# Optimization experiments

Hardware: AMD Instinct MI355X
Metric: run time of the kernel (lower is better)

Reference implementation:

```python
import jax, jax.numpy as jnp
import numpy as np


def setup_inputs() -> dict:
    key = jax.random.key(0)
    ks = jax.random.split(key, 6)
    B, S, D, H, K = 16384, 16, 256, 128, 32
    s1 = 1.0 / np.sqrt(D)
    s2 = 1.0 / np.sqrt(H)
    s3 = 1.0 / np.sqrt(K)
    return {
        "x": jax.random.normal(ks[0], (B, D), jnp.float32),
        "W1": jax.random.normal(ks[1], (S, D, H), jnp.float32) * s1,
        "b1": jnp.zeros((S, H), jnp.float32),
        "W2": jax.random.normal(ks[2], (S, H, D), jnp.float32) * s2,
        "b2": jnp.zeros((S, D), jnp.float32),
        "Wc1": jax.random.normal(ks[3], (S, D, K), jnp.float32) * s1,
        "bc1": jnp.zeros((S, K), jnp.float32),
        "Wc2": jax.random.normal(ks[4], (S, K), jnp.float32) * s3,
        "bc2": jnp.zeros((S,), jnp.float32),
        "lam": jnp.ones((S,), jnp.float32) / S,  # lambda_weights init = 1/n_sources
    }


def reference(x, W1, b1, W2, b2, Wc1, bc1, Wc2, bc2, lam):
    # Batched per-source 2-layer MLP: [B,D] x [S,D,H] -> [B,S,H]
    h = jax.nn.relu(jnp.einsum("bd,sdh->bsh", x, W1) + b1[None])
    outs = jnp.einsum("bsh,shd->bsd", h, W2) + b2[None]            # [B,S,D]
    # Confidence net on each source output
    ch = jax.nn.relu(jnp.einsum("bsd,sdk->bsk", outs, Wc1) + bc1[None])
    conf = jax.nn.sigmoid(jnp.einsum("bsk,sk->bs", ch, Wc2) + bc2[None])  # [B,S]
    # Weighted, normalized combination
    cw = lam[None, :] * conf                                        # [B,S]
    cw = cw / (cw.sum(axis=1, keepdims=True) + 1e-6)
    out = jnp.einsum("bsd,bs->bd", outs, cw)                        # [B,D]
    return out
```

## Files before the change

### kernel.cpp

```cpp
#include <hip/hip_runtime.h>
#include <math.h>

#define S_N 16
#define D_N 256
#define H_N 128
#define K_N 32
#define BT  64
#define B_N 16384

typedef __attribute__((ext_vector_type(8))) short bf16x8;
typedef __attribute__((ext_vector_type(4))) short bf16x4;
typedef __attribute__((ext_vector_type(4))) float f32x4;
typedef __attribute__((ext_vector_type(16))) float f32x16;

#define MFMA16(a, b, c) __builtin_amdgcn_mfma_f32_16x16x32_bf16(a, b, c, 0, 0, 0)
#define MFMA32(a, b, c) __builtin_amdgcn_mfma_f32_32x32x16_bf16(a, b, c, 0, 0, 0)
#define SWZ(r) ((unsigned)(((r) & 15) << 4))

static __device__ __forceinline__ unsigned short f2bf(float f) {
  union { float f; unsigned u; } v; v.f = f;
  unsigned r = v.u + 0x7FFFu + ((v.u >> 16) & 1u);
  return (unsigned short)(r >> 16);
}

__global__ __launch_bounds__(256)
void lsi_prep(const float* __restrict__ W1, const float* __restrict__ W2,
              const float* __restrict__ Wc1, const float* __restrict__ b2,
              const float* __restrict__ bc1,
              unsigned short* __restrict__ W1t,
              unsigned short* __restrict__ W2t,
              unsigned short* __restrict__ Wft,
              float* __restrict__ bcf)
{
  const int bid = blockIdx.x;
  if (bid < 1024) {
    __shared__ float t[32][33];
    const float* src; unsigned short* dst; int R, C, r0, c0;
    if (bid < 512) {
      int s = bid >> 5, tt = bid & 31;
      R = 256; C = 128; r0 = (tt >> 2) * 32; c0 = (tt & 3) * 32;
      src = W1 + (size_t)s * 256 * 128; dst = W1t + (size_t)s * 128 * 256;
    } else {
      int s = (bid - 512) >> 5, tt = (bid - 512) & 31;
      R = 128; C = 256; r0 = (tt >> 3) * 32; c0 = (tt & 7) * 32;
      src = W2 + (size_t)s * 128 * 256; dst = W2t + (size_t)s * 256 * 128;
    }
    int li = threadIdx.x >> 5, lj = threadIdx.x & 31;
    #pragma unroll
    for (int i = 0; i < 4; ++i)
      t[li + i * 8][lj] = src[(size_t)(r0 + li + i * 8) * C + c0 + lj];
    __syncthreads();
    #pragma unroll
    for (int i = 0; i < 4; ++i)
      dst[(size_t)(c0 + li + i * 8) * R + r0 + lj] = f2bf(t[lj][li + i * 8]);
    return;
  }
  const int q  = bid - 1024;
  const int s  = q >> 3, hb = q & 7;
  const int t  = threadIdx.x;
  const int hh = hb * 16 + (t >> 4);
  const int kb = (t & 15) * 2;
  const float* w2r = W2 + ((size_t)s * H_N + hh) * D_N;
  const float* wc1 = Wc1 + (size_t)s * D_N * K_N;
  float a0 = 0.f, a1 = 0.f;
  for (int d = 0; d < D_N; ++d) {
    float wv = w2r[d];
    a0 = fmaf(wv, wc1[d * K_N + kb], a0);
    a1 = fmaf(wv, wc1[d * K_N + kb + 1], a1);
  }
  Wft[((size_t)s * K_N + kb) * H_N + hh]     = f2bf(a0);
  Wft[((size_t)s * K_N + kb + 1) * H_N + hh] = f2bf(a1);
  if (hb == 0 && t < K_N) {
    float a = bc1[s * K_N + t];
    for (int d = 0; d < D_N; ++d)
      a = fmaf(b2[s * D_N + d], wc1[d * K_N + t], a);
    bcf[s * K_N + t] = a;
  }
}

__global__ __launch_bounds__(512, 2)
void lsi_main(const float* __restrict__ x,
              const float* __restrict__ b1,
              const float* __restrict__ b2,
              const float* __restrict__ Wc2,
              const float* __restrict__ bc2,
              const float* __restrict__ lam,
              const unsigned short* __restrict__ W1t,
              const unsigned short* __restrict__ W2t,
              const unsigned short* __restrict__ Wft,
              const float* __restrict__ bcf,
              float* __restrict__ out)
{
  __shared__ __align__(16) unsigned short x_lds[BT * D_N];
  __shared__ __align__(16) unsigned short h_lds[2][BT * H_N];
  __shared__ float cw_lds[2][BT];
  __shared__ float wsum_lds[BT];

  const int tid = threadIdx.x;
  const int w   = tid >> 6;
  const int l   = tid & 63;
  const int l31 = l & 31;
  const int hi  = l >> 5;
  const int l15 = l & 15;
  const int g   = l >> 4;
  const int b0  = blockIdx.x * BT;
  const int bt1 = w >> 2;
  const int ct1 = w & 3;

  {
    int row = tid >> 3;
    int c0  = (tid & 7) * 32;
    const float* xr = x + (size_t)(b0 + row) * D_N + c0;
    #pragma unroll
    for (int cc = 0; cc < 4; ++cc) {
      float4 f0 = *(const float4*)(xr + cc * 8);
      float4 f1 = *(const float4*)(xr + cc * 8 + 4);
      bf16x8 u;
      u[0] = f2bf(f0.x); u[1] = f2bf(f0.y); u[2] = f2bf(f0.z); u[3] = f2bf(f0.w);
      u[4] = f2bf(f1.x); u[5] = f2bf(f1.y); u[6] = f2bf(f1.z); u[7] = f2bf(f1.w);
      unsigned off = (unsigned)(row * 512 + (c0 + cc * 8) * 2) ^ SWZ(row);
      *(bf16x8*)((char*)x_lds + off) = u;
    }
  }
  if (tid < BT) wsum_lds[tid] = 0.f;

  f32x16 out_acc[2], acc2[2];
  #pragma unroll
  for (int i = 0; i < 16; ++i) {
    out_acc[0][i] = 0.f; out_acc[1][i] = 0.f;
  }

  auto do_gemm1 = [&](int s, unsigned short* hw) {
    const int brow = bt1 * 32 + l31;
    f32x16 a1a, a1b;
    #pragma unroll
    for (int i = 0; i < 16; ++i) { a1a[i] = 0.f; a1b[i] = 0.f; }
    const unsigned short* A1 = W1t + ((size_t)s * H_N + ct1 * 32 + l31) * D_N + hi * 8;
    const unsigned xbase = (unsigned)(brow * 512 + hi * 16);
    #pragma unroll
    for (int kf = 0; kf < 16; kf += 2) {
      bf16x8 aw0 = *(const bf16x8*)(A1 + kf * 16);
      bf16x8 aw1 = *(const bf16x8*)(A1 + kf * 16 + 16);
      bf16x8 bx0 = *(const bf16x8*)((const char*)x_lds + ((xbase + kf * 32) ^ SWZ(brow)));
      bf16x8 bx1 = *(const bf16x8*)((const char*)x_lds + ((xbase + kf * 32 + 32) ^ SWZ(brow)));
      a1a = MFMA32(aw0, bx0, a1a);
      a1b = MFMA32(aw1, bx1, a1b);
    }
    #pragma unroll
    for (int q = 0; q < 4; ++q) {
      f32x4 b4 = *(const f32x4*)(b1 + s * H_N + ct1 * 32 + q * 8 + hi * 4);
      bf16x4 hv;
      #pragma unroll
      for (int i = 0; i < 4; ++i)
        hv[i] = (short)f2bf(fmaxf(a1a[q * 4 + i] + a1b[q * 4 + i] + b4[i], 0.f));
      unsigned off = (unsigned)(brow * 256 + (ct1 * 32 + q * 8 + hi * 4) * 2) ^ SWZ(brow);
      *(bf16x4*)((char*)hw + off) = hv;
    }
  };

  __syncthreads();
  do_gemm1(0, h_lds[0]);
  __syncthreads();

  for (int s = 0; s < S_N; ++s) {
    const unsigned short* hr = (const unsigned short*)h_lds[s & 1];

    if (s > 0) {
      float cw0 = cw_lds[(s - 1) & 1][l31];
      float cw1 = cw_lds[(s - 1) & 1][32 + l31];
      #pragma unroll
      for (int r = 0; r < 16; ++r) {
        out_acc[0][r] += cw0 * acc2[0][r];
        out_acc[1][r] += cw1 * acc2[1][r];
      }
    }

    if (s + 1 < S_N) do_gemm1(s + 1, h_lds[(s + 1) & 1]);

    if (w < 4) {
      const int crow = w * 16 + l15;
      f32x4 c3a = (f32x4){0.f, 0.f, 0.f, 0.f};
      f32x4 c3b = (f32x4){0.f, 0.f, 0.f, 0.f};
      const unsigned short* Af = Wft + ((size_t)s * K_N + l15) * H_N + g * 8;
      const unsigned cb = (unsigned)(crow * 256 + g * 16);
      #pragma unroll
      for (int ks = 0; ks < 4; ++ks) {
        bf16x8 hb = *(const bf16x8*)((const char*)hr + ((cb + ks * 64) ^ SWZ(crow)));
        c3a = MFMA16(*(const bf16x8*)(Af + ks * 32), hb, c3a);
        c3b = MFMA16(*(const bf16x8*)(Af + 16 * H_N + ks * 32), hb, c3b);
      }
      float zz = 0.f;
      {
        f32x4 bcf4 = *(const f32x4*)(bcf + s * K_N + g * 4);
        f32x4 wc4  = *(const f32x4*)(Wc2 + s * K_N + g * 4);
        #pragma unroll
        for (int i = 0; i < 4; ++i)
          zz += fmaxf(c3a[i] + bcf4[i], 0.f) * wc4[i];
        bcf4 = *(const f32x4*)(bcf + s * K_N + 16 + g * 4);
        wc4  = *(const f32x4*)(Wc2 + s * K_N + 16 + g * 4);
        #pragma unroll
        for (int i = 0; i < 4; ++i)
          zz += fmaxf(c3b[i] + bcf4[i], 0.f) * wc4[i];
      }
      zz += __shfl_xor(zz, 16);
      zz += __shfl_xor(zz, 32);
      if (l < 16) {
        float cv = lam[s] / (1.f + __expf(-(zz + bc2[s])));
        cw_lds[s & 1][w * 16 + l] = cv;
        wsum_lds[w * 16 + l] += cv;
      }
    }

    #pragma unroll
    for (int i = 0; i < 16; ++i) { acc2[0][i] = 0.f; acc2[1][i] = 0.f; }
    {
      const unsigned short* A2 = W2t + ((size_t)s * D_N + w * 32 + l31) * H_N + hi * 8;
      const unsigned hb0 = (unsigned)(l31 * 256 + hi * 16);
      const unsigned hb1 = (unsigned)((32 + l31) * 256 + hi * 16);
      #pragma unroll
      for (int kf = 0; kf < 8; ++kf) {
        bf16x8 aw = *(const bf16x8*)(A2 + kf * 16);
        bf16x8 h0 = *(const bf16x8*)((const char*)hr + ((hb0 + kf * 32) ^ SWZ(l31)));
        bf16x8 h1 = *(const bf16x8*)((const char*)hr + ((hb1 + kf * 32) ^ SWZ(l31)));
        acc2[0] = MFMA32(aw, h0, acc2[0]);
        acc2[1] = MFMA32(aw, h1, acc2[1]);
      }
      #pragma unroll
      for (int q = 0; q < 4; ++q) {
        f32x4 b24 = *(const f32x4*)(b2 + s * D_N + w * 32 + q * 8 + hi * 4);
        #pragma unroll
        for (int i = 0; i < 4; ++i) {
          acc2[0][q * 4 + i] += b24[i];
          acc2[1][q * 4 + i] += b24[i];
        }
      }
    }
    __syncthreads();
  }

  {
    float cw0 = cw_lds[(S_N - 1) & 1][l31];
    float cw1 = cw_lds[(S_N - 1) & 1][32 + l31];
    float wi0 = 1.f / (wsum_lds[l31] + 1e-6f);
    float wi1 = 1.f / (wsum_lds[32 + l31] + 1e-6f);
    #pragma unroll
    for (int r = 0; r < 16; ++r) {
      out_acc[0][r] = (out_acc[0][r] + cw0 * acc2[0][r]) * wi0;
      out_acc[1][r] = (out_acc[1][r] + cw1 * acc2[1][r]) * wi1;
    }
  }
  {
    float* tb = (w < 4 ? (float*)x_lds : (float*)h_lds) + (w & 3) * 1152;
    #pragma unroll
    for (int t = 0; t < 2; ++t) {
      __syncthreads();
      #pragma unroll
      for (int q = 0; q < 4; ++q) {
        f32x4 v;
        #pragma unroll
        for (int i = 0; i < 4; ++i) v[i] = out_acc[t][q * 4 + i];
        *(f32x4*)(tb + l31 * 36 + q * 8 + hi * 4) = v;
      }
      __syncthreads();
      #pragma unroll
      for (int p = 0; p < 2; ++p) {
        int row = (l >> 2) + p * 16;
        f32x4 v0 = *(const f32x4*)(tb + row * 36 + (l & 3) * 8);
        f32x4 v1 = *(const f32x4*)(tb + row * 36 + (l & 3) * 8 + 4);
        float* op = out + (size_t)(b0 + t * 32 + row) * D_N + w * 32 + (l & 3) * 8;
        *(f32x4*)op = v0;
        *(f32x4*)(op + 4) = v1;
      }
    }
  }
}

extern "C" void kernel_launch(void* const* d_in, const int* in_sizes, int n_in,
                              void* d_out, int out_size, void* d_ws, size_t ws_size,
                              hipStream_t stream) {
  const float* x   = (const float*)d_in[0];
  const float* W1  = (const float*)d_in[1];
  const float* b1  = (const float*)d_in[2];
  const float* W2  = (const float*)d_in[3];
  const float* b2  = (const float*)d_in[4];
  const float* Wc1 = (const float*)d_in[5];
  const float* bc1 = (const float*)d_in[6];
  const float* Wc2 = (const float*)d_in[7];
  const float* bc2 = (const float*)d_in[8];
  const float* lam = (const float*)d_in[9];
  float* out = (float*)d_out;

  unsigned short* W1t = (unsigned short*)d_ws;
  unsigned short* W2t = W1t + (size_t)S_N * H_N * D_N;
  unsigned short* Wft = W2t + (size_t)S_N * D_N * H_N;
  float* bcf = (float*)(Wft + (size_t)S_N * K_N * H_N);

  lsi_prep<<<dim3(1152), dim3(256), 0, stream>>>(W1, W2, Wc1, b2, bc1,
                                                 W1t, W2t, Wft, bcf);
  lsi_main<<<dim3(B_N / BT), dim3(512), 0, stream>>>(x, b1, b2, Wc2, bc2, lam,
                                                     W1t, W2t, Wft, bcf, out);
}
```

Before: 137.8 us.

## Fold confidence weights into hidden activations and split sources across two blocks

Scales the hidden activations h by each row's confidence weight before the second GEMM, so the weighted sum over sources accumulates straight into the MFMA output instead of through a separate FMA pass. The b2 bias contribution is added once at the end using stored per-source weights. Tiles shrink to 32 rows with 256-thread blocks, and when workspace allows, the 16 sources are split across two blocks whose partial sums and weight totals are merged by a new combine kernel. This gives more parallelism and occupancy, at the cost of an extra bf16 rounding of the scaled h, extra barriers per source, and the write and read of two full fp32 partial outputs.

```diff
diff --git a/kernel.cpp b/kernel.cpp
--- a/kernel.cpp
+++ b/kernel.cpp
@@ -5,7 +5,7 @@
 #define D_N 256
 #define H_N 128
 #define K_N 32
-#define BT  64
+#define BT  32
 #define B_N 16384
 
 typedef __attribute__((ext_vector_type(8))) short bf16x8;
@@ -21,6 +21,10 @@
   union { float f; unsigned u; } v; v.f = f;
   unsigned r = v.u + 0x7FFFu + ((v.u >> 16) & 1u);
   return (unsigned short)(r >> 16);
+}
+static __device__ __forceinline__ float bf2f(unsigned short u) {
+  union { unsigned u; float f; } v; v.u = ((unsigned)u) << 16;
+  return v.f;
 }
 
 __global__ __launch_bounds__(256)
@@ -78,7 +82,8 @@
   }
 }
 
-__global__ __launch_bounds__(512, 2)
+template<int SPLIT>
+__global__ __launch_bounds__(256, 4)
 void lsi_main(const float* __restrict__ x,
               const float* __restrict__ b1,
               const float* __restrict__ b2,
@@ -89,11 +94,13 @@
               const unsigned short* __restrict__ W2t,
               const unsigned short* __restrict__ Wft,
               const float* __restrict__ bcf,
-              float* __restrict__ out)
+              float* __restrict__ outp,
+              float* __restrict__ pwsum)
 {
   __shared__ __align__(16) unsigned short x_lds[BT * D_N];
   __shared__ __align__(16) unsigned short h_lds[2][BT * H_N];
-  __shared__ float cw_lds[2][BT];
+  __shared__ float zp_lds[2][BT];
+  __shared__ float cwh[16][BT];
   __shared__ float wsum_lds[BT];
 
   const int tid = threadIdx.x;
@@ -103,9 +110,11 @@
   const int hi  = l >> 5;
   const int l15 = l & 15;
   const int g   = l >> 4;
-  const int b0  = blockIdx.x * BT;
-  const int bt1 = w >> 2;
-  const int ct1 = w & 3;
+
+  int rb, half, s0, ns;
+  if (SPLIT) { rb = blockIdx.x & 511; half = blockIdx.x >> 9; s0 = half * 8; ns = 8; }
+  else       { rb = blockIdx.x;       half = 0;               s0 = 0;        ns = 16; }
+  const int b0 = rb * BT;
 
   {
     int row = tid >> 3;
@@ -124,141 +133,135 @@
   }
   if (tid < BT) wsum_lds[tid] = 0.f;
 
-  f32x16 out_acc[2], acc2[2];
+  f32x16 oa0, oa1;
   #pragma unroll
-  for (int i = 0; i < 16; ++i) {
-    out_acc[0][i] = 0.f; out_acc[1][i] = 0.f;
-  }
+  for (int i = 0; i < 16; ++i) { oa0[i] = 0.f; oa1[i] = 0.f; }
 
   auto do_gemm1 = [&](int s, unsigned short* hw) {
-    const int brow = bt1 * 32 + l31;
-    f32x16 a1a, a1b;
-    #pragma unroll
-    for (int i = 0; i < 16; ++i) { a1a[i] = 0.f; a1b[i] = 0.f; }
-    const unsigned short* A1 = W1t + ((size_t)s * H_N + ct1 * 32 + l31) * D_N + hi * 8;
-    const unsigned xbase = (unsigned)(brow * 512 + hi * 16);
-    #pragma unroll
-    for (int kf = 0; kf < 16; kf += 2) {
-      bf16x8 aw0 = *(const bf16x8*)(A1 + kf * 16);
-      bf16x8 aw1 = *(const bf16x8*)(A1 + kf * 16 + 16);
-      bf16x8 bx0 = *(const bf16x8*)((const char*)x_lds + ((xbase + kf * 32) ^ SWZ(brow)));
-      bf16x8 bx1 = *(const bf16x8*)((const char*)x_lds + ((xbase + kf * 32 + 32) ^ SWZ(brow)));
-      a1a = MFMA32(aw0, bx0, a1a);
-      a1b = MFMA32(aw1, bx1, a1b);
+    f32x16 a1;
+    #pragma unroll
+    for (int i = 0; i < 16; ++i) a1[i] = 0.f;
+    const unsigned short* A1 = W1t + ((size_t)s * H_N + w * 32 + l31) * D_N + hi * 8;
+    #pragma unroll
+    for (int kf = 0; kf < 16; ++kf) {
+      bf16x8 aw = *(const bf16x8*)(A1 + kf * 16);
+      bf16x8 bx = *(const bf16x8*)((const char*)x_lds +
+                    ((unsigned)(l31 * 512 + kf * 32 + hi * 16) ^ SWZ(l31)));
+      a1 = MFMA32(aw, bx, a1);
     }
     #pragma unroll
     for (int q = 0; q < 4; ++q) {
-      f32x4 b4 = *(const f32x4*)(b1 + s * H_N + ct1 * 32 + q * 8 + hi * 4);
+      f32x4 b4 = *(const f32x4*)(b1 + s * H_N + w * 32 + q * 8 + hi * 4);
       bf16x4 hv;
       #pragma unroll
       for (int i = 0; i < 4; ++i)
-        hv[i] = (short)f2bf(fmaxf(a1a[q * 4 + i] + a1b[q * 4 + i] + b4[i], 0.f));
-      unsigned off = (unsigned)(brow * 256 + (ct1 * 32 + q * 8 + hi * 4) * 2) ^ SWZ(brow);
+        hv[i] = (short)f2bf(fmaxf(a1[q * 4 + i] + b4[i], 0.f));
+      unsigned off = (unsigned)(l31 * 256 + (w * 32 + q * 8 + hi * 4) * 2) ^ SWZ(l31);
       *(bf16x4*)((char*)hw + off) = hv;
     }
   };
 
   __syncthreads();
-  do_gemm1(0, h_lds[0]);
+  do_gemm1(s0, h_lds[0]);
   __syncthreads();
 
-  for (int s = 0; s < S_N; ++s) {
-    const unsigned short* hr = (const unsigned short*)h_lds[s & 1];
-
-    if (s > 0) {
-      float cw0 = cw_lds[(s - 1) & 1][l31];
-      float cw1 = cw_lds[(s - 1) & 1][32 + l31];
-      #pragma unroll
-      for (int r = 0; r < 16; ++r) {
-        out_acc[0][r] += cw0 * acc2[0][r];
-        out_acc[1][r] += cw1 * acc2[1][r];
-      }
-    }
-
-    if (s + 1 < S_N) do_gemm1(s + 1, h_lds[(s + 1) & 1]);
-
-    if (w < 4) {
-      const int crow = w * 16 + l15;
-      f32x4 c3a = (f32x4){0.f, 0.f, 0.f, 0.f};
-      f32x4 c3b = (f32x4){0.f, 0.f, 0.f, 0.f};
-      const unsigned short* Af = Wft + ((size_t)s * K_N + l15) * H_N + g * 8;
-      const unsigned cb = (unsigned)(crow * 256 + g * 16);
+  for (int si = 0; si < ns; ++si) {
+    const int s = s0 + si;
+    const unsigned short* hr = (const unsigned short*)h_lds[si & 1];
+
+    if (si + 1 < ns) do_gemm1(s + 1, h_lds[(si + 1) & 1]);
+    {
+      const int bt = w >> 1, kt = w & 1;
+      f32x4 c3 = (f32x4){0.f, 0.f, 0.f, 0.f};
+      const unsigned short* Af = Wft + ((size_t)s * K_N + kt * 16 + l15) * H_N + g * 8;
       #pragma unroll
       for (int ks = 0; ks < 4; ++ks) {
-        bf16x8 hb = *(const bf16x8*)((const char*)hr + ((cb + ks * 64) ^ SWZ(crow)));
-        c3a = MFMA16(*(const bf16x8*)(Af + ks * 32), hb, c3a);
-        c3b = MFMA16(*(const bf16x8*)(Af + 16 * H_N + ks * 32), hb, c3b);
-      }
+        int brow = bt * 16 + l15;
+        bf16x8 hb = *(const bf16x8*)((const char*)hr +
+                      ((unsigned)(brow * 256 + ks * 64 + g * 16) ^ SWZ(brow)));
+        c3 = MFMA16(*(const bf16x8*)(Af + ks * 32), hb, c3);
+      }
+      f32x4 bc4 = *(const f32x4*)(bcf + s * K_N + kt * 16 + g * 4);
+      f32x4 wc4 = *(const f32x4*)(Wc2 + s * K_N + kt * 16 + g * 4);
       float zz = 0.f;
-      {
-        f32x4 bcf4 = *(const f32x4*)(bcf + s * K_N + g * 4);
-        f32x4 wc4  = *(const f32x4*)(Wc2 + s * K_N + g * 4);
-        #pragma unroll
-        for (int i = 0; i < 4; ++i)
-          zz += fmaxf(c3a[i] + bcf4[i], 0.f) * wc4[i];
-        bcf4 = *(const f32x4*)(bcf + s * K_N + 16 + g * 4);
-        wc4  = *(const f32x4*)(Wc2 + s * K_N + 16 + g * 4);
-        #pragma unroll
-        for (int i = 0; i < 4; ++i)
-          zz += fmaxf(c3b[i] + bcf4[i], 0.f) * wc4[i];
-      }
+      #pragma unroll
+      for (int i = 0; i < 4; ++i)
+        zz += fmaxf(c3[i] + bc4[i], 0.f) * wc4[i];
       zz += __shfl_xor(zz, 16);
       zz += __shfl_xor(zz, 32);
-      if (l < 16) {
-        float cv = lam[s] / (1.f + __expf(-(zz + bc2[s])));
-        cw_lds[s & 1][w * 16 + l] = cv;
-        wsum_lds[w * 16 + l] += cv;
-      }
-    }
-
-    #pragma unroll
-    for (int i = 0; i < 16; ++i) { acc2[0][i] = 0.f; acc2[1][i] = 0.f; }
+      if (l < 16) zp_lds[kt][bt * 16 + l] = zz;
+    }
+    __syncthreads();
+
     {
-      const unsigned short* A2 = W2t + ((size_t)s * D_N + w * 32 + l31) * H_N + hi * 8;
-      const unsigned hb0 = (unsigned)(l31 * 256 + hi * 16);
-      const unsigned hb1 = (unsigned)((32 + l31) * 256 + hi * 16);
+      unsigned short* hm = h_lds[si & 1];
+      const int r  = tid >> 3;
+      const int c0 = (tid & 7) * 32;
+      float cv = lam[s] / (1.f + __expf(-(zp_lds[0][r] + zp_lds[1][r] + bc2[s])));
+      unsigned off0 = (unsigned)(r * 256 + c0) ^ SWZ(r);
+      unsigned off1 = (unsigned)(r * 256 + c0 + 16) ^ SWZ(r);
+      bf16x8 v0 = *(const bf16x8*)((const char*)hm + off0);
+      bf16x8 v1 = *(const bf16x8*)((const char*)hm + off1);
+      #pragma unroll
+      for (int j = 0; j < 8; ++j) {
+        v0[j] = (short)f2bf(bf2f((unsigned short)v0[j]) * cv);
+        v1[j] = (short)f2bf(bf2f((unsigned short)v1[j]) * cv);
+      }
+      *(bf16x8*)((char*)hm + off0) = v0;
+      *(bf16x8*)((char*)hm + off1) = v1;
+      if ((tid & 7) == 0) {
+        wsum_lds[r] += cv;
+        cwh[si][r] = cv;
+      }
+    }
+    __syncthreads();
+
+    {
+      const unsigned short* A2 = W2t + ((size_t)s * D_N + w * 64 + l31) * H_N + hi * 8;
       #pragma unroll
       for (int kf = 0; kf < 8; ++kf) {
-        bf16x8 aw = *(const bf16x8*)(A2 + kf * 16);
-        bf16x8 h0 = *(const bf16x8*)((const char*)hr + ((hb0 + kf * 32) ^ SWZ(l31)));
-        bf16x8 h1 = *(const bf16x8*)((const char*)hr + ((hb1 + kf * 32) ^ SWZ(l31)));
-        acc2[0] = MFMA32(aw, h0, acc2[0]);
-        acc2[1] = MFMA32(aw, h1, acc2[1]);
-      }
-      #pragma unroll
-      for (int q = 0; q < 4; ++q) {
-        f32x4 b24 = *(const f32x4*)(b2 + s * D_N + w * 32 + q * 8 + hi * 4);
-        #pragma unroll
-        for (int i = 0; i < 4; ++i) {
-          acc2[0][q * 4 + i] += b24[i];
-          acc2[1][q * 4 + i] += b24[i];
-        }
+        bf16x8 hb = *(const bf16x8*)((const char*)hr +
+                      ((unsigned)(l31 * 256 + kf * 32 + hi * 16) ^ SWZ(l31)));
+        oa0 = MFMA32(*(const bf16x8*)(A2 + kf * 16), hb, oa0);
+        oa1 = MFMA32(*(const bf16x8*)(A2 + 32 * H_N + kf * 16), hb, oa1);
       }
     }
     __syncthreads();
   }
 
+  #pragma unroll
+  for (int q = 0; q < 4; ++q) {
+    const int dc0 = w * 64 + q * 8 + hi * 4;
+    for (int si = 0; si < ns; ++si) {
+      const float c = cwh[si][l31];
+      f32x4 ba = *(const f32x4*)(b2 + (s0 + si) * D_N + dc0);
+      f32x4 bb = *(const f32x4*)(b2 + (s0 + si) * D_N + dc0 + 32);
+      #pragma unroll
+      for (int i = 0; i < 4; ++i) {
+        oa0[q * 4 + i] += c * ba[i];
+        oa1[q * 4 + i] += c * bb[i];
+      }
+    }
+  }
+  if (!SPLIT) {
+    const float winv = 1.f / (wsum_lds[l31] + 1e-6f);
+    #pragma unroll
+    for (int i = 0; i < 16; ++i) { oa0[i] *= winv; oa1[i] *= winv; }
+  }
+
   {
-    float cw0 = cw_lds[(S_N - 1) & 1][l31];
-    float cw1 = cw_lds[(S_N - 1) & 1][32 + l31];
-    float wi0 = 1.f / (wsum_lds[l31] + 1e-6f);
-    float wi1 = 1.f / (wsum_lds[32 + l31] + 1e-6f);
-    #pragma unroll
-    for (int r = 0; r < 16; ++r) {
-      out_acc[0][r] = (out_acc[0][r] + cw0 * acc2[0][r]) * wi0;
-      out_acc[1][r] = (out_acc[1][r] + cw1 * acc2[1][r]) * wi1;
-    }
-  }
-  {
-    float* tb = (w < 4 ? (float*)x_lds : (float*)h_lds) + (w & 3) * 1152;
-    #pragma unroll
-    for (int t = 0; t < 2; ++t) {
+    float* tb = (w < 2) ? ((float*)x_lds + w * 1152)
+                        : ((float*)h_lds + (w - 2) * 1152);
+    float* po = outp + (SPLIT ? (size_t)half * B_N * D_N : 0);
+    #pragma unroll
+    for (int ct = 0; ct < 2; ++ct) {
       __syncthreads();
       #pragma unroll
       for (int q = 0; q < 4; ++q) {
         f32x4 v;
         #pragma unroll
-        for (int i = 0; i < 4; ++i) v[i] = out_acc[t][q * 4 + i];
+        for (int i = 0; i < 4; ++i)
+          v[i] = ct ? oa1[q * 4 + i] : oa0[q * 4 + i];
         *(f32x4*)(tb + l31 * 36 + q * 8 + hi * 4) = v;
       }
       __syncthreads();
@@ -267,12 +270,29 @@
         int row = (l >> 2) + p * 16;
         f32x4 v0 = *(const f32x4*)(tb + row * 36 + (l & 3) * 8);
         f32x4 v1 = *(const f32x4*)(tb + row * 36 + (l & 3) * 8 + 4);
-        float* op = out + (size_t)(b0 + t * 32 + row) * D_N + w * 32 + (l & 3) * 8;
+        float* op = po + (size_t)(b0 + row) * D_N + w * 64 + ct * 32 + (l & 3) * 8;
         *(f32x4*)op = v0;
         *(f32x4*)(op + 4) = v1;
       }
     }
   }
+  if (SPLIT && tid < BT) pwsum[half * B_N + b0 + tid] = wsum_lds[tid];
+}
+
+__global__ __launch_bounds__(256)
+void lsi_combine(const float* __restrict__ pout, const float* __restrict__ pwsum,
+                 float* __restrict__ out)
+{
+  size_t i4 = ((size_t)blockIdx.x * 256 + threadIdx.x) * 4;
+  int row = (int)(i4 >> 8);
+  f32x4 a = *(const f32x4*)(pout + i4);
+  f32x4 b = *(const f32x4*)(pout + (size_t)B_N * D_N + i4);
+  float ws = pwsum[row] + pwsum[B_N + row];
+  float inv = 1.f / (ws + 1e-6f);
+  f32x4 r;
+  #pragma unroll
+  for (int i = 0; i < 4; ++i) r[i] = (a[i] + b[i]) * inv;
+  *(f32x4*)(out + i4) = r;
 }
 
 extern "C" void kernel_launch(void* const* d_in, const int* in_sizes, int n_in,
@@ -293,10 +313,19 @@
   unsigned short* W1t = (unsigned short*)d_ws;
   unsigned short* W2t = W1t + (size_t)S_N * H_N * D_N;
   unsigned short* Wft = W2t + (size_t)S_N * D_N * H_N;
-  float* bcf = (float*)(Wft + (size_t)S_N * K_N * H_N);
+  float* bcf   = (float*)(Wft + (size_t)S_N * K_N * H_N);
+  float* pwsum = bcf + S_N * K_N;
+  float* pout  = pwsum + 2 * B_N;
+  size_t need = (size_t)((char*)(pout + (size_t)2 * B_N * D_N) - (char*)d_ws);
 
   lsi_prep<<<dim3(1152), dim3(256), 0, stream>>>(W1, W2, Wc1, b2, bc1,
                                                  W1t, W2t, Wft, bcf);
-  lsi_main<<<dim3(B_N / BT), dim3(512), 0, stream>>>(x, b1, b2, Wc2, bc2, lam,
-                                                     W1t, W2t, Wft, bcf, out);
-}
+  if (ws_size >= need) {
+    lsi_main<1><<<dim3(1024), dim3(256), 0, stream>>>(x, b1, b2, Wc2, bc2, lam,
+                                                      W1t, W2t, Wft, bcf, pout, pwsum);
+    lsi_combine<<<dim3((B_N * D_N) / 1024), dim3(256), 0, stream>>>(pout, pwsum, out);
+  } else {
+    lsi_main<0><<<dim3(512), dim3(256), 0, stream>>>(x, b1, b2, Wc2, bc2, lam,
+                                                     W1t, W2t, Wft, bcf, out, nullptr);
+  }
+}
```

After: 181.4 us. 31.6% more time.
